# Kernel tuning notes

Hardware: AMD Instinct MI355X
Metric: run time of the kernel (lower is better)

The kernel has to match this reference:

```python
import jax, jax.numpy as jnp
import numpy as np

D_MODEL = 1024
N_HEADS = 16
HEAD_DIM = D_MODEL // N_HEADS
BATCH = 4
SEQ = 2048
NEG_INF = -1000000000.0  # matches torch masked_fill value in source


def setup_inputs() -> dict:
    key = jax.random.key(0)
    ks = jax.random.split(key, 5)
    scale = 1.0 / np.sqrt(D_MODEL)
    x = jax.random.normal(ks[0], (BATCH, SEQ, D_MODEL), dtype=jnp.float32)
    wq = jax.random.normal(ks[1], (D_MODEL, D_MODEL), dtype=jnp.float32) * scale
    wk = jax.random.normal(ks[2], (D_MODEL, D_MODEL), dtype=jnp.float32) * scale
    wv = jax.random.normal(ks[3], (D_MODEL, D_MODEL), dtype=jnp.float32) * scale
    wo = jax.random.normal(ks[4], (D_MODEL, D_MODEL), dtype=jnp.float32) * scale
    return {"x": x, "wq": wq, "wk": wk, "wv": wv, "wo": wo}


def reference(x, wq, wk, wv, wo):
    b, s, d = x.shape
    # projections (weights applied as x @ W^T, matching nn-style Linear weights)
    q = jnp.einsum('bsd,ed->bse', x, wq).reshape(b, s, N_HEADS, HEAD_DIM).transpose(0, 2, 1, 3)
    k = jnp.einsum('bsd,ed->bse', x, wk).reshape(b, s, N_HEADS, HEAD_DIM).transpose(0, 2, 1, 3)
    v = jnp.einsum('bsd,ed->bse', x, wv).reshape(b, s, N_HEADS, HEAD_DIM).transpose(0, 2, 1, 3)
    # scaled dot-product scores [b, h, s, s]
    scores = jnp.einsum('bhqd,bhkd->bhqk', q, k) / jnp.sqrt(jnp.float32(HEAD_DIM))
    # causal mask: positions strictly above diagonal masked with -1e9
    causal = jnp.triu(jnp.ones((s, s), dtype=bool), k=1)
    scores = jnp.where(causal[None, None], jnp.float32(NEG_INF), scores)
    attn = jax.nn.softmax(scores, axis=-1)
    out = jnp.einsum('bhqk,bhkd->bhqd', attn, v)
    out = out.transpose(0, 2, 1, 3).reshape(b, s, d)
    return jnp.einsum('bsd,ed->bse', out, wo)
```

## Files before the change

### kernel.cpp

```cpp
#include <hip/hip_runtime.h>
#include <hip/hip_bf16.h>

typedef __hip_bfloat16 bf16;
typedef __attribute__((ext_vector_type(8))) short short8;
typedef __attribute__((ext_vector_type(4))) short short4_t;
typedef __attribute__((ext_vector_type(4))) float f32x4;
typedef unsigned int u32;

#define MFMA16(a, b, c) __builtin_amdgcn_mfma_f32_16x16x32_bf16(a, b, c, 0, 0, 0)

#if __has_builtin(__builtin_amdgcn_exp2f)
#define EXP2(x) __builtin_amdgcn_exp2f(x)
#else
#define EXP2(x) __expf((x) * 0.6931471805599453f)
#endif

static constexpr int S_ = 2048, D_ = 1024, M_ = 8192;
static constexpr size_t SZ = (size_t)M_ * D_;
static constexpr size_t WSZ = (size_t)D_ * D_;
static constexpr float QSCALE = 0.125f * 1.4426950408889634f;

__device__ __forceinline__ void gload16(void* lds, const void* g) {
  __builtin_amdgcn_global_load_lds((const __attribute__((address_space(1))) void*)g,
                                   (__attribute__((address_space(3))) void*)lds, 16, 0, 0);
}

__device__ __forceinline__ short4_t cvt4(const float4 v) {
  short4_t r;
  r[0] = (short)__bfloat16_as_ushort(__float2bfloat16(v.x));
  r[1] = (short)__bfloat16_as_ushort(__float2bfloat16(v.y));
  r[2] = (short)__bfloat16_as_ushort(__float2bfloat16(v.z));
  r[3] = (short)__bfloat16_as_ushort(__float2bfloat16(v.w));
  return r;
}

__device__ __forceinline__ u32 pk2(float a, float b) {
  return (u32)__bfloat16_as_ushort(__float2bfloat16(a)) |
         ((u32)__bfloat16_as_ushort(__float2bfloat16(b)) << 16);
}

__global__ __launch_bounds__(256) void cvt_f32_bf16(const float* __restrict__ in,
                                                    bf16* __restrict__ out, int n4) {
  int stride = gridDim.x * 256;
  for (int i = blockIdx.x * 256 + threadIdx.x; i < n4; i += stride) {
    float4 v = ((const float4*)in)[i];
    *(short4_t*)&out[(size_t)i * 4] = cvt4(v);
  }
}

__global__ __launch_bounds__(256) void cvt_all(const float* __restrict__ x,
                                               const float* __restrict__ wq,
                                               const float* __restrict__ wk,
                                               const float* __restrict__ wv,
                                               const float* __restrict__ wo,
                                               bf16* __restrict__ xb,
                                               bf16* __restrict__ wqkv,
                                               bf16* __restrict__ wob, int nseg) {
  const int X4 = (int)(SZ / 4);
  const int per = 1 << 18;
  int total = X4 + nseg * per;
  for (int i = blockIdx.x * 256 + threadIdx.x; i < total; i += gridDim.x * 256) {
    const float* s;
    bf16* d;
    int off;
    if (i < X4) {
      s = x; d = xb; off = i;
    } else {
      int j = i - X4;
      int seg = j >> 18;
      off = j & (per - 1);
      s = (seg == 0) ? wq : (seg == 1) ? wk : (seg == 2) ? wv : wo;
      d = (seg < 3) ? (wqkv + ((size_t)seg << 20)) : wob;
    }
    float4 v = ((const float4*)s)[off];
    *(short4_t*)&d[(size_t)off * 4] = cvt4(v);
  }
}

__global__ __launch_bounds__(256) void qkv_gemm(const bf16* __restrict__ A,
                                                const bf16* __restrict__ Wqkv,
                                                bf16* __restrict__ QKV) {
  __shared__ __align__(16) bf16 lA[128 * 32];
  __shared__ __align__(16) bf16 lB[128 * 32];
  const int tid = threadIdx.x, lane = tid & 63, w = tid >> 6;
  const int wr = w >> 1, wc = w & 1;
  const int m0 = blockIdx.x * 128;
  const int mat = blockIdx.y >> 3, n0 = (blockIdx.y & 7) * 128;
  const bf16* W = Wqkv + (size_t)mat * WSZ;
  bf16* C = QKV + (size_t)mat * SZ;
  const int l15 = lane & 15, lg = lane >> 4;

  f32x4 zero = {0.f, 0.f, 0.f, 0.f};
  f32x4 acc[4][4];
#pragma unroll
  for (int i = 0; i < 4; i++)
#pragma unroll
    for (int j = 0; j < 4; j++) acc[i][j] = zero;

  for (int kt = 0; kt < 32; ++kt) {
    const int k0 = kt * 32;
#pragma unroll
    for (int i = 0; i < 2; ++i) {
      int c = i * 256 + tid;
      int row = c >> 2, col = (c & 3) * 8;
      gload16(&lA[c * 8], &A[(size_t)(m0 + row) * 1024 + k0 + col]);
      gload16(&lB[c * 8], &W[(size_t)(n0 + row) * 1024 + k0 + col]);
    }
    __syncthreads();

    short8 af[4], bfr[4];
#pragma unroll
    for (int mi = 0; mi < 4; mi++)
      af[mi] = *(const short8*)&lA[(wr * 64 + mi * 16 + l15) * 32 + lg * 8];
#pragma unroll
    for (int ni = 0; ni < 4; ni++)
      bfr[ni] = *(const short8*)&lB[(wc * 64 + ni * 16 + l15) * 32 + lg * 8];
    if (mat == 2) {
#pragma unroll
      for (int mi = 0; mi < 4; mi++)
#pragma unroll
        for (int ni = 0; ni < 4; ni++) acc[mi][ni] = MFMA16(bfr[ni], af[mi], acc[mi][ni]);
    } else {
#pragma unroll
      for (int mi = 0; mi < 4; mi++)
#pragma unroll
        for (int ni = 0; ni < 4; ni++) acc[mi][ni] = MFMA16(af[mi], bfr[ni], acc[mi][ni]);
    }
    __syncthreads();
  }

  if (mat == 2) {
#pragma unroll
    for (int mi = 0; mi < 4; mi++)
#pragma unroll
      for (int ni = 0; ni < 4; ni++)
#pragma unroll
        for (int r = 0; r < 4; r++) {
          int m = m0 + wr * 64 + mi * 16 + l15;
          int n = n0 + wc * 64 + ni * 16 + lg * 4 + r;
          int b = m >> 11, s = m & 2047, h = n >> 6, dh = n & 63;
          size_t idx = ((size_t)((b << 4) + h) * 64 + dh) * 2048 + s;
          C[idx] = __float2bfloat16(acc[mi][ni][r]);
        }
  } else {
    const float scale = (mat == 0) ? QSCALE : 1.0f;
#pragma unroll
    for (int mi = 0; mi < 4; mi++)
#pragma unroll
      for (int ni = 0; ni < 4; ni++)
#pragma unroll
        for (int r = 0; r < 4; r++) {
          int m = m0 + wr * 64 + mi * 16 + lg * 4 + r;
          int n = n0 + wc * 64 + ni * 16 + l15;
          int b = m >> 11, s = m & 2047, h = n >> 6, dh = n & 63;
          size_t idx = ((size_t)((b << 4) + h) * 2048 + s) * 64 + dh;
          C[idx] = __float2bfloat16(acc[mi][ni][r] * scale);
        }
  }
}

__global__ __launch_bounds__(256) void gemm_out(const bf16* __restrict__ A,
                                                const bf16* __restrict__ W,
                                                float* __restrict__ C) {
  __shared__ __align__(16) bf16 lA[128 * 32];
  __shared__ __align__(16) bf16 lB[128 * 32];
  const int tid = threadIdx.x, lane = tid & 63, w = tid >> 6;
  const int wr = w >> 1, wc = w & 1;
  const int m0 = blockIdx.x * 128, n0 = blockIdx.y * 128;
  const int l15 = lane & 15, lg = lane >> 4;

  f32x4 zero = {0.f, 0.f, 0.f, 0.f};
  f32x4 acc[4][4];
#pragma unroll
  for (int i = 0; i < 4; i++)
#pragma unroll
    for (int j = 0; j < 4; j++) acc[i][j] = zero;

  for (int kt = 0; kt < 32; ++kt) {
    const int k0 = kt * 32;
#pragma unroll
    for (int i = 0; i < 2; ++i) {
      int c = i * 256 + tid;
      int row = c >> 2, col = (c & 3) * 8;
      gload16(&lA[c * 8], &A[(size_t)(m0 + row) * 1024 + k0 + col]);
      gload16(&lB[c * 8], &W[(size_t)(n0 + row) * 1024 + k0 + col]);
    }
    __syncthreads();

    short8 af[4], bfr[4];
#pragma unroll
    for (int mi = 0; mi < 4; mi++)
      af[mi] = *(const short8*)&lA[(wr * 64 + mi * 16 + l15) * 32 + lg * 8];
#pragma unroll
    for (int ni = 0; ni < 4; ni++)
      bfr[ni] = *(const short8*)&lB[(wc * 64 + ni * 16 + l15) * 32 + lg * 8];
#pragma unroll
    for (int mi = 0; mi < 4; mi++)
#pragma unroll
      for (int ni = 0; ni < 4; ni++) acc[mi][ni] = MFMA16(af[mi], bfr[ni], acc[mi][ni]);
    __syncthreads();
  }

#pragma unroll
  for (int mi = 0; mi < 4; mi++)
#pragma unroll
    for (int ni = 0; ni < 4; ni++)
#pragma unroll
      for (int r = 0; r < 4; r++) {
        int m = m0 + wr * 64 + mi * 16 + lg * 4 + r;
        int n = n0 + wc * 64 + ni * 16 + l15;
        C[(size_t)m * 1024 + n] = acc[mi][ni][r];
      }
}

__global__ __launch_bounds__(256, 3) void attn_fwd(const bf16* __restrict__ Q,
                                                   const bf16* __restrict__ K,
                                                   const bf16* __restrict__ Vt,
                                                   bf16* __restrict__ O) {
  __shared__ __align__(16) bf16 lK[2][64 * 64];
  __shared__ __align__(16) bf16 lV[2][64 * 64];
  __shared__ __align__(16) bf16 lP[4][32 * 64];
  const int tid = threadIdx.x, lane = tid & 63, w = tid >> 6;
  const int l15 = lane & 15, lg = lane >> 4;
  const int bh = blockIdx.x;
  const int qb = 15 - blockIdx.y;
  const int q0 = qb * 128 + w * 32;
  const bf16* Qb = Q + (size_t)bh * S_ * 64;
  const bf16* Kb = K + (size_t)bh * S_ * 64;
  const bf16* Vb = Vt + (size_t)bh * 64 * S_;
  bf16* Pw = lP[w];

  short8 qf[2][2];
#pragma unroll
  for (int mi = 0; mi < 2; mi++)
#pragma unroll
    for (int kd = 0; kd < 2; kd++)
      qf[mi][kd] = *(const short8*)&Qb[(size_t)(q0 + mi * 16 + l15) * 64 + kd * 32 + lg * 8];

  f32x4 zero = {0.f, 0.f, 0.f, 0.f};
  f32x4 acc[2][4];
  float mr[2], lr[2];
#pragma unroll
  for (int mi = 0; mi < 2; mi++) {
    mr[mi] = -1e9f;
    lr[mi] = 0.f;
#pragma unroll
    for (int ni = 0; ni < 4; ni++) acc[mi][ni] = zero;
  }

  const int nch = (qb + 1) * 2;

#define STAGE(buf, c)                                                                   \
  {                                                                                     \
    _Pragma("unroll") for (int i = 0; i < 2; ++i) {                                     \
      int t2 = i * 256 + tid;                                                           \
      int row = t2 >> 3;                                                                \
      int cb = ((t2 & 7) * 16) ^ ((row & 7) << 4);                                      \
      gload16((char*)lK[buf] + t2 * 16, (const char*)Kb + (size_t)((c) * 64 + row) * 128 + cb); \
      gload16((char*)lV[buf] + t2 * 16, (const char*)Vb + (size_t)row * 4096 + (size_t)(c) * 128 + cb); \
    }                                                                                   \
  }

  STAGE(0, 0);
  int cur = 0;
  for (int c = 0; c < nch; ++c) {
    __builtin_amdgcn_s_barrier();
    if (c + 1 < nch) {
      STAGE(cur ^ 1, c + 1);
      asm volatile("s_waitcnt vmcnt(4)" ::: "memory");
    } else {
      asm volatile("s_waitcnt vmcnt(0)" ::: "memory");
    }
    __builtin_amdgcn_s_barrier();

    if (c * 64 <= q0 + 31) {
      const int c0 = c * 64;
      f32x4 sc[2][4];
#pragma unroll
      for (int mi = 0; mi < 2; mi++)
#pragma unroll
        for (int ch = 0; ch < 4; ch++) sc[mi][ch] = zero;
      const char* Kc = (const char*)lK[cur];
      __builtin_amdgcn_s_setprio(1);
#pragma unroll
      for (int kd = 0; kd < 2; ++kd)
#pragma unroll
        for (int ch = 0; ch < 4; ++ch) {
          short8 kf = *(const short8*)(Kc + (ch * 16 + l15) * 128 + ((kd * 64 + lg * 16) ^ ((l15 & 7) << 4)));
          sc[0][ch] = MFMA16(kf, qf[0][kd], sc[0][ch]);
          sc[1][ch] = MFMA16(kf, qf[1][kd], sc[1][ch]);
        }
      __builtin_amdgcn_s_setprio(0);

      if (c0 + 63 > q0) {
#pragma unroll
        for (int mi = 0; mi < 2; mi++) {
          int q = q0 + mi * 16 + l15;
#pragma unroll
          for (int ch = 0; ch < 4; ch++)
#pragma unroll
            for (int r = 0; r < 4; r++) {
              int kv = c0 + ch * 16 + lg * 4 + r;
              if (kv > q) sc[mi][ch][r] = -1e9f;
            }
        }
      }

#pragma unroll
      for (int mi = 0; mi < 2; mi++) {
        float v0 = fmaxf(fmaxf(sc[mi][0][0], sc[mi][0][1]), fmaxf(sc[mi][0][2], sc[mi][0][3]));
        float v1 = fmaxf(fmaxf(sc[mi][1][0], sc[mi][1][1]), fmaxf(sc[mi][1][2], sc[mi][1][3]));
        float v2 = fmaxf(fmaxf(sc[mi][2][0], sc[mi][2][1]), fmaxf(sc[mi][2][2], sc[mi][2][3]));
        float v3 = fmaxf(fmaxf(sc[mi][3][0], sc[mi][3][1]), fmaxf(sc[mi][3][2], sc[mi][3][3]));
        float vmax = fmaxf(fmaxf(v0, v1), fmaxf(v2, v3));
        vmax = fmaxf(vmax, __shfl_xor(vmax, 16));
        vmax = fmaxf(vmax, __shfl_xor(vmax, 32));
        if (!__all(vmax <= mr[mi] + 8.f)) {
          float mn = fmaxf(mr[mi], vmax);
          float corr = EXP2(mr[mi] - mn);
          mr[mi] = mn;
          lr[mi] *= corr;
#pragma unroll
          for (int r = 0; r < 4; r++) {
            float cr = __shfl(corr, (lane & 48) | (((lane >> 4) << 2) + r));
#pragma unroll
            for (int ni = 0; ni < 4; ni++) acc[mi][ni][r] *= cr;
          }
        }
        float ps0 = 0.f, ps1 = 0.f, ps2 = 0.f, ps3 = 0.f;
#pragma unroll
        for (int ch = 0; ch < 4; ch++) {
          float p0 = EXP2(sc[mi][ch][0] - mr[mi]);
          float p1 = EXP2(sc[mi][ch][1] - mr[mi]);
          float p2 = EXP2(sc[mi][ch][2] - mr[mi]);
          float p3 = EXP2(sc[mi][ch][3] - mr[mi]);
          sc[mi][ch][0] = p0; sc[mi][ch][1] = p1; sc[mi][ch][2] = p2; sc[mi][ch][3] = p3;
          ps0 += p0; ps1 += p1; ps2 += p2; ps3 += p3;
        }
        float ps = (ps0 + ps1) + (ps2 + ps3);
        ps += __shfl_xor(ps, 16);
        ps += __shfl_xor(ps, 32);
        lr[mi] += ps;
        int row = mi * 16 + l15;
        char* Pb = (char*)Pw + row * 128;
        int sw = (row & 7) << 4;
#pragma unroll
        for (int ch = 0; ch < 4; ch++) {
          u32 d0 = pk2(sc[mi][ch][0], sc[mi][ch][1]);
          u32 d1 = pk2(sc[mi][ch][2], sc[mi][ch][3]);
          uint2 dd = {d0, d1};
          *(uint2*)(Pb + ((ch * 32 + lg * 8) ^ sw)) = dd;
        }
      }

      asm volatile("s_waitcnt lgkmcnt(0)" ::: "memory");
      const char* Vc = (const char*)lV[cur];
      __builtin_amdgcn_s_setprio(1);
#pragma unroll
      for (int kd = 0; kd < 2; ++kd) {
        short8 pf[2];
#pragma unroll
        for (int mi = 0; mi < 2; mi++)
          pf[mi] = *(const short8*)((const char*)Pw + (mi * 16 + l15) * 128 +
                                    ((kd * 64 + lg * 16) ^ ((l15 & 7) << 4)));
#pragma unroll
        for (int ni = 0; ni < 4; ++ni) {
          short8 vf = *(const short8*)(Vc + (ni * 16 + l15) * 128 + ((kd * 64 + lg * 16) ^ ((l15 & 7) << 4)));
          acc[0][ni] = MFMA16(pf[0], vf, acc[0][ni]);
          acc[1][ni] = MFMA16(pf[1], vf, acc[1][ni]);
        }
      }
      __builtin_amdgcn_s_setprio(0);
    }
    cur ^= 1;
  }
#undef STAGE

  const int b = bh >> 4, h = bh & 15;
#pragma unroll
  for (int mi = 0; mi < 2; mi++) {
    float lrr[4];
#pragma unroll
    for (int r = 0; r < 4; r++)
      lrr[r] = __shfl(lr[mi], (lane & 48) | (((lane >> 4) << 2) + r));
#pragma unroll
    for (int ni = 0; ni < 4; ni++)
#pragma unroll
      for (int r = 0; r < 4; r++) {
        int q = q0 + mi * 16 + lg * 4 + r;
        size_t idx = ((size_t)(b * 2048 + q)) * 1024 + h * 64 + ni * 16 + l15;
        O[idx] = __float2bfloat16(acc[mi][ni][r] / lrr[r]);
      }
  }
}

extern "C" void kernel_launch(void* const* d_in, const int* in_sizes, int n_in,
                              void* d_out, int out_size, void* d_ws, size_t ws_size,
                              hipStream_t stream) {
  const float* x = (const float*)d_in[0];
  const float* wq = (const float*)d_in[1];
  const float* wk = (const float*)d_in[2];
  const float* wv = (const float*)d_in[3];
  const float* wo = (const float*)d_in[4];
  float* out = (float*)d_out;

  bf16* xb = (bf16*)d_ws;
  bf16* Qw = xb + SZ;
  bf16* AO = xb;
  bf16* wqkv = (bf16*)d_out;

  const bool ws_has_wo = ws_size >= (4 * SZ + WSZ) * sizeof(bf16);
  bf16* wob = ws_has_wo ? (xb + 4 * SZ) : Qw;

  dim3 blk(256);
  hipLaunchKernelGGL(cvt_all, dim3(2048), blk, 0, stream, x, wq, wk, wv, wo, xb, wqkv, wob,
                     ws_has_wo ? 4 : 3);
  hipLaunchKernelGGL(qkv_gemm, dim3(64, 24), blk, 0, stream, xb, wqkv, Qw);
  hipLaunchKernelGGL(attn_fwd, dim3(64, 16), blk, 0, stream, Qw, Qw + SZ, Qw + 2 * SZ, AO);
  if (!ws_has_wo)
    hipLaunchKernelGGL(cvt_f32_bf16, dim3(512), blk, 0, stream, wo, wob, (int)(WSZ / 4));
  hipLaunchKernelGGL(gemm_out, dim3(64, 8), blk, 0, stream, AO, wob, out);
}
```

Measured before the change: 259.7 us.

## Double-buffer GEMM LDS tiles and vectorize epilogue stores

Both projection GEMMs now use two LDS buffers, prefetching the next K tile with async global-to-LDS loads while the current tile is computed. Waits use explicit vmcnt counts and raw barriers. MFMA operand order is swapped so each lane holds four consecutive output columns, which lets the epilogue write packed bf16x4 or float4 values instead of scalar stores. This aims to hide global load latency and cut store instruction count, at the cost of double the LDS per block and reliance on hand-counted vmcnt.

```diff
diff --git a/kernel.cpp b/kernel.cpp
--- a/kernel.cpp
+++ b/kernel.cpp
@@ -77,11 +77,21 @@
   }
 }
 
+#define GSTAGE(buf, kt)                                                              \
+  {                                                                                  \
+    _Pragma("unroll") for (int i_ = 0; i_ < 2; ++i_) {                               \
+      int c_ = i_ * 256 + tid;                                                       \
+      int row_ = c_ >> 2, col_ = (c_ & 3) * 8;                                       \
+      gload16(&lA[buf][c_ * 8], &A[(size_t)(m0 + row_) * 1024 + (kt) * 32 + col_]);  \
+      gload16(&lB[buf][c_ * 8], &W[(size_t)(n0 + row_) * 1024 + (kt) * 32 + col_]);  \
+    }                                                                                \
+  }
+
 __global__ __launch_bounds__(256) void qkv_gemm(const bf16* __restrict__ A,
                                                 const bf16* __restrict__ Wqkv,
                                                 bf16* __restrict__ QKV) {
-  __shared__ __align__(16) bf16 lA[128 * 32];
-  __shared__ __align__(16) bf16 lB[128 * 32];
+  __shared__ __align__(16) bf16 lA[2][128 * 32];
+  __shared__ __align__(16) bf16 lB[2][128 * 32];
   const int tid = threadIdx.x, lane = tid & 63, w = tid >> 6;
   const int wr = w >> 1, wc = w & 1;
   const int m0 = blockIdx.x * 128;
@@ -97,73 +107,72 @@
 #pragma unroll
     for (int j = 0; j < 4; j++) acc[i][j] = zero;
 
+  GSTAGE(0, 0);
+  int cur = 0;
   for (int kt = 0; kt < 32; ++kt) {
-    const int k0 = kt * 32;
-#pragma unroll
-    for (int i = 0; i < 2; ++i) {
-      int c = i * 256 + tid;
-      int row = c >> 2, col = (c & 3) * 8;
-      gload16(&lA[c * 8], &A[(size_t)(m0 + row) * 1024 + k0 + col]);
-      gload16(&lB[c * 8], &W[(size_t)(n0 + row) * 1024 + k0 + col]);
-    }
-    __syncthreads();
+    if (kt + 1 < 32) {
+      GSTAGE(cur ^ 1, kt + 1);
+      asm volatile("s_waitcnt vmcnt(4)" ::: "memory");
+    } else {
+      asm volatile("s_waitcnt vmcnt(0)" ::: "memory");
+    }
+    __builtin_amdgcn_s_barrier();
 
     short8 af[4], bfr[4];
 #pragma unroll
     for (int mi = 0; mi < 4; mi++)
-      af[mi] = *(const short8*)&lA[(wr * 64 + mi * 16 + l15) * 32 + lg * 8];
+      af[mi] = *(const short8*)&lA[cur][(wr * 64 + mi * 16 + l15) * 32 + lg * 8];
 #pragma unroll
     for (int ni = 0; ni < 4; ni++)
-      bfr[ni] = *(const short8*)&lB[(wc * 64 + ni * 16 + l15) * 32 + lg * 8];
+      bfr[ni] = *(const short8*)&lB[cur][(wc * 64 + ni * 16 + l15) * 32 + lg * 8];
     if (mat == 2) {
 #pragma unroll
       for (int mi = 0; mi < 4; mi++)
 #pragma unroll
+        for (int ni = 0; ni < 4; ni++) acc[mi][ni] = MFMA16(af[mi], bfr[ni], acc[mi][ni]);
+    } else {
+#pragma unroll
+      for (int mi = 0; mi < 4; mi++)
+#pragma unroll
         for (int ni = 0; ni < 4; ni++) acc[mi][ni] = MFMA16(bfr[ni], af[mi], acc[mi][ni]);
-    } else {
-#pragma unroll
-      for (int mi = 0; mi < 4; mi++)
-#pragma unroll
-        for (int ni = 0; ni < 4; ni++) acc[mi][ni] = MFMA16(af[mi], bfr[ni], acc[mi][ni]);
-    }
-    __syncthreads();
+    }
+    __builtin_amdgcn_s_barrier();
+    cur ^= 1;
   }
 
   if (mat == 2) {
 #pragma unroll
     for (int mi = 0; mi < 4; mi++)
 #pragma unroll
-      for (int ni = 0; ni < 4; ni++)
-#pragma unroll
-        for (int r = 0; r < 4; r++) {
-          int m = m0 + wr * 64 + mi * 16 + l15;
-          int n = n0 + wc * 64 + ni * 16 + lg * 4 + r;
-          int b = m >> 11, s = m & 2047, h = n >> 6, dh = n & 63;
-          size_t idx = ((size_t)((b << 4) + h) * 64 + dh) * 2048 + s;
-          C[idx] = __float2bfloat16(acc[mi][ni][r]);
-        }
+      for (int ni = 0; ni < 4; ni++) {
+        int mB = m0 + wr * 64 + mi * 16 + lg * 4;
+        int n = n0 + wc * 64 + ni * 16 + l15;
+        int b = mB >> 11, s = mB & 2047, h = n >> 6, dh = n & 63;
+        uint2 dd = {pk2(acc[mi][ni][0], acc[mi][ni][1]),
+                    pk2(acc[mi][ni][2], acc[mi][ni][3])};
+        *(uint2*)&C[((size_t)((b << 4) + h) * 64 + dh) * 2048 + s] = dd;
+      }
   } else {
     const float scale = (mat == 0) ? QSCALE : 1.0f;
 #pragma unroll
     for (int mi = 0; mi < 4; mi++)
 #pragma unroll
-      for (int ni = 0; ni < 4; ni++)
-#pragma unroll
-        for (int r = 0; r < 4; r++) {
-          int m = m0 + wr * 64 + mi * 16 + lg * 4 + r;
-          int n = n0 + wc * 64 + ni * 16 + l15;
-          int b = m >> 11, s = m & 2047, h = n >> 6, dh = n & 63;
-          size_t idx = ((size_t)((b << 4) + h) * 2048 + s) * 64 + dh;
-          C[idx] = __float2bfloat16(acc[mi][ni][r] * scale);
-        }
+      for (int ni = 0; ni < 4; ni++) {
+        int m = m0 + wr * 64 + mi * 16 + l15;
+        int nB = n0 + wc * 64 + ni * 16 + lg * 4;
+        int b = m >> 11, s = m & 2047, h = nB >> 6, dh = nB & 63;
+        uint2 dd = {pk2(acc[mi][ni][0] * scale, acc[mi][ni][1] * scale),
+                    pk2(acc[mi][ni][2] * scale, acc[mi][ni][3] * scale)};
+        *(uint2*)&C[((size_t)((b << 4) + h) * 2048 + s) * 64 + dh] = dd;
+      }
   }
 }
 
 __global__ __launch_bounds__(256) void gemm_out(const bf16* __restrict__ A,
                                                 const bf16* __restrict__ W,
                                                 float* __restrict__ C) {
-  __shared__ __align__(16) bf16 lA[128 * 32];
-  __shared__ __align__(16) bf16 lB[128 * 32];
+  __shared__ __align__(16) bf16 lA[2][128 * 32];
+  __shared__ __align__(16) bf16 lB[2][128 * 32];
   const int tid = threadIdx.x, lane = tid & 63, w = tid >> 6;
   const int wr = w >> 1, wc = w & 1;
   const int m0 = blockIdx.x * 128, n0 = blockIdx.y * 128;
@@ -176,41 +185,41 @@
 #pragma unroll
     for (int j = 0; j < 4; j++) acc[i][j] = zero;
 
+  GSTAGE(0, 0);
+  int cur = 0;
   for (int kt = 0; kt < 32; ++kt) {
-    const int k0 = kt * 32;
-#pragma unroll
-    for (int i = 0; i < 2; ++i) {
-      int c = i * 256 + tid;
-      int row = c >> 2, col = (c & 3) * 8;
-      gload16(&lA[c * 8], &A[(size_t)(m0 + row) * 1024 + k0 + col]);
-      gload16(&lB[c * 8], &W[(size_t)(n0 + row) * 1024 + k0 + col]);
-    }
-    __syncthreads();
+    if (kt + 1 < 32) {
+      GSTAGE(cur ^ 1, kt + 1);
+      asm volatile("s_waitcnt vmcnt(4)" ::: "memory");
+    } else {
+      asm volatile("s_waitcnt vmcnt(0)" ::: "memory");
+    }
+    __builtin_amdgcn_s_barrier();
 
     short8 af[4], bfr[4];
 #pragma unroll
     for (int mi = 0; mi < 4; mi++)
-      af[mi] = *(const short8*)&lA[(wr * 64 + mi * 16 + l15) * 32 + lg * 8];
+      af[mi] = *(const short8*)&lA[cur][(wr * 64 + mi * 16 + l15) * 32 + lg * 8];
 #pragma unroll
     for (int ni = 0; ni < 4; ni++)
-      bfr[ni] = *(const short8*)&lB[(wc * 64 + ni * 16 + l15) * 32 + lg * 8];
+      bfr[ni] = *(const short8*)&lB[cur][(wc * 64 + ni * 16 + l15) * 32 + lg * 8];
 #pragma unroll
     for (int mi = 0; mi < 4; mi++)
 #pragma unroll
-      for (int ni = 0; ni < 4; ni++) acc[mi][ni] = MFMA16(af[mi], bfr[ni], acc[mi][ni]);
-    __syncthreads();
+      for (int ni = 0; ni < 4; ni++) acc[mi][ni] = MFMA16(bfr[ni], af[mi], acc[mi][ni]);
+    __builtin_amdgcn_s_barrier();
+    cur ^= 1;
   }
 
 #pragma unroll
   for (int mi = 0; mi < 4; mi++)
 #pragma unroll
-    for (int ni = 0; ni < 4; ni++)
-#pragma unroll
-      for (int r = 0; r < 4; r++) {
-        int m = m0 + wr * 64 + mi * 16 + lg * 4 + r;
-        int n = n0 + wc * 64 + ni * 16 + l15;
-        C[(size_t)m * 1024 + n] = acc[mi][ni][r];
-      }
+    for (int ni = 0; ni < 4; ni++) {
+      int m = m0 + wr * 64 + mi * 16 + l15;
+      int nB = n0 + wc * 64 + ni * 16 + lg * 4;
+      float4 v = {acc[mi][ni][0], acc[mi][ni][1], acc[mi][ni][2], acc[mi][ni][3]};
+      *(float4*)&C[(size_t)m * 1024 + nB] = v;
+    }
 }
 
 __global__ __launch_bounds__(256, 3) void attn_fwd(const bf16* __restrict__ Q,
```

New measurement: 279.1 us. +7.5%, slower.
